# Kernel optimization log

Hardware: AMD Instinct MI355X
Metric: run time of the kernel (lower is better)

Reference implementation:

```python
import jax, jax.numpy as jnp
import numpy as np

OUT_H = 7  # _height_
OUT_W = 7  # _width_


def _bin_ids(start, end, size, nbins):
    # Per-pixel segment id along one spatial axis; id == nbins marks pixels outside the ROI.
    # Mirrors TF: step = int(region / nbins); bin i covers [i*step, (i+1)*step), last bin extends to region end.
    step = ((end - start).astype(jnp.float32) / nbins).astype(jnp.int32)
    idx = jnp.arange(size)
    rel = idx - start
    b = jnp.minimum(rel // jnp.maximum(step, 1), nbins - 1)
    b = jnp.where(step > 0, b, nbins - 1)  # degenerate step==0: everything valid falls in last bin
    valid = (rel >= 0) & (idx < end)
    return jnp.where(valid, b, nbins)


def _pool_one(fmap, roi):
    # fmap: [H, W, C], roi: [4] = (h_min, w_min, h_max, w_max) relative coords
    H, W, C = fmap.shape
    h0 = (H * roi[0]).astype(jnp.int32)
    w0 = (W * roi[1]).astype(jnp.int32)
    h1 = (H * roi[2]).astype(jnp.int32)
    w1 = (W * roi[3]).astype(jnp.int32)
    colb = _bin_ids(w0, w1, W, OUT_W)  # [W]
    rowb = _bin_ids(h0, h1, H, OUT_H)  # [H]
    # Max is separable over rows/cols: pool columns first, then rows.
    tmp = jax.ops.segment_max(jnp.transpose(fmap, (1, 0, 2)), colb, num_segments=OUT_W + 1)[:OUT_W]  # [OUT_W, H, C]
    out = jax.ops.segment_max(jnp.transpose(tmp, (1, 0, 2)), rowb, num_segments=OUT_H + 1)[:OUT_H]   # [OUT_H, OUT_W, C]
    return out


def _roi_pool(feature_map, rois):
    per_image = jax.vmap(_pool_one, in_axes=(None, 0))  # over ROIs
    return jax.vmap(per_image)(feature_map, rois)       # over batch -> [B, R, OUT_H, OUT_W, C]


def setup_inputs() -> dict:
    key = jax.random.key(0)
    k1, k2, k3 = jax.random.split(key, 3)
    B, H, W, C, R = 4, 56, 56, 256, 64
    feature_map = jax.random.normal(k1, (B, H, W, C), dtype=jnp.float32)
    # valid ROIs: (h_min, w_min) in [0, 0.45), extent in [0.30, 0.55) so every 7x7 bin is non-empty
    starts = jax.random.uniform(k2, (B, R, 2), minval=0.0, maxval=0.45, dtype=jnp.float32)
    lens = jax.random.uniform(k3, (B, R, 2), minval=0.30, maxval=0.55, dtype=jnp.float32)
    rois = jnp.concatenate([starts, jnp.minimum(starts + lens, 1.0)], axis=-1)  # [B, R, 4]
    return {"feature_map": feature_map, "rois": rois}


def reference(feature_map, rois):
    return _roi_pool(feature_map, rois)
```

## Files before the change

kernel.cpp:

```cpp
#include <hip/hip_runtime.h>


#define OUT_H 7
#define OUT_W 7
#define NBIN (OUT_H * OUT_W)
#define NB 4
#define NR 64
#define NH 56
#define NW 56
#define NC 256
#define C4 (NC / 4)

#define BLKS_PER_XCD_SLOT 392

typedef float v4f __attribute__((ext_vector_type(4)));

__device__ __forceinline__ v4f vmax4(v4f a, v4f b) {
    v4f r;
    r.x = fmaxf(a.x, b.x);
    r.y = fmaxf(a.y, b.y);
    r.z = fmaxf(a.z, b.z);
    r.w = fmaxf(a.w, b.w);
    return r;
}

__global__ __launch_bounds__(256) void roi_pool_kernel(
    const float* __restrict__ fmap,
    const float* __restrict__ rois,
    float* __restrict__ out)
{
    const int blk  = blockIdx.x;
    const int xcd  = blk & 7;
    const int b    = xcd >> 1;
    const int wid  = threadIdx.x >> 6;
    const int lane = threadIdx.x & 63;

    const int work = ((xcd & 1) * BLKS_PER_XCD_SLOT) + (blk >> 3);
    const int gbin = work * 4 + wid;
    const int r    = gbin / NBIN;
    const int bin  = gbin - r * NBIN;
    const int oi   = bin / OUT_W;
    const int oj   = bin - oi * OUT_W;

    const float* roi = rois + (size_t)(b * NR + r) * 4;
    const float r0 = roi[0], r1 = roi[1], r2 = roi[2], r3 = roi[3];
    const int h0 = (int)((float)NH * r0);
    const int w0 = (int)((float)NW * r1);
    const int h1 = (int)((float)NH * r2);
    const int w1 = (int)((float)NW * r3);

    const int hstep = (int)((float)(h1 - h0) / (float)OUT_H);
    const int wstep = (int)((float)(w1 - w0) / (float)OUT_W);

    int rlo, rhi, clo, chi;
    if (hstep >= 1) {
        rlo = h0 + oi * hstep;
        rhi = (oi < OUT_H - 1) ? (rlo + hstep) : h1;
    } else {
        rlo = (oi == OUT_H - 1) ? h0 : 0;
        rhi = (oi == OUT_H - 1) ? h1 : 0;
    }
    if (wstep >= 1) {
        clo = w0 + oj * wstep;
        chi = (oj < OUT_W - 1) ? (clo + wstep) : w1;
    } else {
        clo = (oj == OUT_W - 1) ? w0 : 0;
        chi = (oj == OUT_W - 1) ? w1 : 0;
    }

    const v4f* base =
        (const v4f*)(fmap + (size_t)b * NH * NW * NC) + lane;

    const v4f ninf = (v4f){-INFINITY, -INFINITY, -INFINITY, -INFINITY};
    v4f acc0 = ninf, acc1 = ninf, acc2 = ninf, acc3 = ninf;

    int h = rlo;
    for (; h + 1 < rhi; h += 2) {
        const v4f* r0p = base + (size_t)(h * NW) * C4;
        const v4f* r1p = r0p + (size_t)NW * C4;
        int w = clo;
        for (; w + 1 < chi; w += 2) {
            v4f a = r0p[(size_t)w * C4];
            v4f bb = r0p[(size_t)(w + 1) * C4];
            v4f c = r1p[(size_t)w * C4];
            v4f d = r1p[(size_t)(w + 1) * C4];
            acc0 = vmax4(acc0, a);
            acc1 = vmax4(acc1, bb);
            acc2 = vmax4(acc2, c);
            acc3 = vmax4(acc3, d);
        }
        if (w < chi) {
            v4f a = r0p[(size_t)w * C4];
            v4f c = r1p[(size_t)w * C4];
            acc0 = vmax4(acc0, a);
            acc2 = vmax4(acc2, c);
        }
    }
    if (h < rhi) {
        const v4f* r0p = base + (size_t)(h * NW) * C4;
        int w = clo;
        for (; w + 1 < chi; w += 2) {
            v4f a = r0p[(size_t)w * C4];
            v4f bb = r0p[(size_t)(w + 1) * C4];
            acc0 = vmax4(acc0, a);
            acc1 = vmax4(acc1, bb);
        }
        if (w < chi) acc0 = vmax4(acc0, r0p[(size_t)w * C4]);
    }

    v4f acc = vmax4(vmax4(acc0, acc1), vmax4(acc2, acc3));

    const size_t obase = ((size_t)((b * NR + r) * NBIN + bin)) * NC;
    v4f* o = (v4f*)(out + obase);
    __builtin_nontemporal_store(acc, o + lane);
}

extern "C" void kernel_launch(void* const* d_in, const int* in_sizes, int n_in,
                              void* d_out, int out_size, void* d_ws, size_t ws_size,
                              hipStream_t stream) {
    const float* fmap = (const float*)d_in[0];
    const float* rois = (const float*)d_in[1];
    float* out = (float*)d_out;

    const int nblocks = NB * NR * NBIN / 4;
    roi_pool_kernel<<<nblocks, 256, 0, stream>>>(fmap, rois, out);
}
```

Measured before the change: 15.73 us.

## Split each ROI bin across four waves with LDS max reduction

Each block now handles a single output bin instead of four. The four waves split that bin's columns, with each wave taking every fourth column, and their partial maxima are combined through shared memory before wave 0 stores the result. The grid grows fourfold, so each wave carries a shorter serial load chain and more memory-level parallelism. In exchange it adds a __syncthreads, LDS traffic and more block launch overhead.

New measurement: 18.44 us. 1.17x slower.

```diff
diff --git a/kernel.cpp b/kernel.cpp
--- a/kernel.cpp
+++ b/kernel.cpp
@@ -11,7 +11,7 @@
 #define NC 256
 #define C4 (NC / 4)
 
-#define BLKS_PER_XCD_SLOT 392
+#define BLKS_PER_XCD_SLOT 1568
 
 typedef float v4f __attribute__((ext_vector_type(4)));
 
@@ -29,6 +29,8 @@
     const float* __restrict__ rois,
     float* __restrict__ out)
 {
+    __shared__ v4f red[3][64];
+
     const int blk  = blockIdx.x;
     const int xcd  = blk & 7;
     const int b    = xcd >> 1;
@@ -36,9 +38,8 @@
     const int lane = threadIdx.x & 63;
 
     const int work = ((xcd & 1) * BLKS_PER_XCD_SLOT) + (blk >> 3);
-    const int gbin = work * 4 + wid;
-    const int r    = gbin / NBIN;
-    const int bin  = gbin - r * NBIN;
+    const int r    = work / NBIN;
+    const int bin  = work - r * NBIN;
     const int oi   = bin / OUT_W;
     const int oj   = bin - oi * OUT_W;
 
@@ -74,45 +75,46 @@
     const v4f ninf = (v4f){-INFINITY, -INFINITY, -INFINITY, -INFINITY};
     v4f acc0 = ninf, acc1 = ninf, acc2 = ninf, acc3 = ninf;
 
+    const int wstart = clo + wid;
+
     int h = rlo;
     for (; h + 1 < rhi; h += 2) {
         const v4f* r0p = base + (size_t)(h * NW) * C4;
         const v4f* r1p = r0p + (size_t)NW * C4;
-        int w = clo;
-        for (; w + 1 < chi; w += 2) {
-            v4f a = r0p[(size_t)w * C4];
-            v4f bb = r0p[(size_t)(w + 1) * C4];
-            v4f c = r1p[(size_t)w * C4];
-            v4f d = r1p[(size_t)(w + 1) * C4];
-            acc0 = vmax4(acc0, a);
-            acc1 = vmax4(acc1, bb);
-            acc2 = vmax4(acc2, c);
-            acc3 = vmax4(acc3, d);
+        int w = wstart;
+        for (; w + 4 < chi; w += 8) {
+            acc0 = vmax4(acc0, r0p[(size_t)w * C4]);
+            acc1 = vmax4(acc1, r0p[(size_t)(w + 4) * C4]);
+            acc2 = vmax4(acc2, r1p[(size_t)w * C4]);
+            acc3 = vmax4(acc3, r1p[(size_t)(w + 4) * C4]);
         }
         if (w < chi) {
-            v4f a = r0p[(size_t)w * C4];
-            v4f c = r1p[(size_t)w * C4];
-            acc0 = vmax4(acc0, a);
-            acc2 = vmax4(acc2, c);
+            acc0 = vmax4(acc0, r0p[(size_t)w * C4]);
+            acc2 = vmax4(acc2, r1p[(size_t)w * C4]);
         }
     }
     if (h < rhi) {
         const v4f* r0p = base + (size_t)(h * NW) * C4;
-        int w = clo;
-        for (; w + 1 < chi; w += 2) {
-            v4f a = r0p[(size_t)w * C4];
-            v4f bb = r0p[(size_t)(w + 1) * C4];
-            acc0 = vmax4(acc0, a);
-            acc1 = vmax4(acc1, bb);
+        int w = wstart;
+        for (; w + 4 < chi; w += 8) {
+            acc0 = vmax4(acc0, r0p[(size_t)w * C4]);
+            acc1 = vmax4(acc1, r0p[(size_t)(w + 4) * C4]);
         }
         if (w < chi) acc0 = vmax4(acc0, r0p[(size_t)w * C4]);
     }
 
     v4f acc = vmax4(vmax4(acc0, acc1), vmax4(acc2, acc3));
 
-    const size_t obase = ((size_t)((b * NR + r) * NBIN + bin)) * NC;
-    v4f* o = (v4f*)(out + obase);
-    __builtin_nontemporal_store(acc, o + lane);
+    if (wid > 0) red[wid - 1][lane] = acc;
+    __syncthreads();
+
+    if (wid == 0) {
+        acc = vmax4(acc, red[0][lane]);
+        acc = vmax4(acc, vmax4(red[1][lane], red[2][lane]));
+        const size_t obase = ((size_t)((b * NR + r) * NBIN + bin)) * NC;
+        v4f* o = (v4f*)(out + obase);
+        __builtin_nontemporal_store(acc, o + lane);
+    }
 }
 
 extern "C" void kernel_launch(void* const* d_in, const int* in_sizes, int n_in,
@@ -122,6 +124,6 @@
     const float* rois = (const float*)d_in[1];
     float* out = (float*)d_out;
 
-    const int nblocks = NB * NR * NBIN / 4;
+    const int nblocks = NB * NR * NBIN;
     roi_pool_kernel<<<nblocks, 256, 0, stream>>>(fmap, rois, out);
 }
```
